# Kernel tuning notes

Measured on AMD Instinct MI355X. Metric: run time of the kernel, lower is better.

Reference implementation:

```python
import jax, jax.numpy as jnp
import numpy as np

SENSOR_H, SENSOR_W = 256, 256
SPP = 16
BATCH, C, H_IMG, W_IMG = 4, 3, 1024, 1024


def setup_inputs() -> dict:
    key = jax.random.key(0)
    k1, k2 = jax.random.split(key)
    img = jax.random.uniform(k1, (BATCH, C, H_IMG, W_IMG), dtype=jnp.float32)
    jitter = jax.random.uniform(k2, (SPP, SENSOR_H, SENSOR_W, 2), dtype=jnp.float32)
    t = jnp.ones((1,), jnp.float32)
    return {"img": img, "t": t, "jitter": jitter}


def deform(pos, t):
    # Analytic per-axis foveation diffeomorphism [-1,1]^2 -> [-1,1]^2:
    #   f(u) = tanh(t*u)/tanh(t), f'(u) = t*(1 - tanh(t*u)^2)/tanh(t)
    # Jacobian is diagonal, so det = f'(x) * f'(y).
    tt = t[0]
    s = jnp.tanh(tt)
    th = jnp.tanh(tt * pos)
    warped = th / s                      # (..., 2)
    dd = tt * (1.0 - th * th) / s        # diagonal Jacobian entries (..., 2)
    det = dd[..., 0] * dd[..., 1]        # (...)
    return warped, det


def grid_sample_border(img, grid):
    # img: (b,c,H,W); grid: (spp,h,w,2) in [-1,1]
    # bilinear, padding_mode='border', align_corners=False (matches F.grid_sample)
    b, c, H, W = img.shape
    gx = (grid[..., 0] + 1.0) * (W / 2.0) - 0.5
    gy = (grid[..., 1] + 1.0) * (H / 2.0) - 0.5
    gx = jnp.clip(gx, 0.0, W - 1.0)
    gy = jnp.clip(gy, 0.0, H - 1.0)
    x0 = jnp.floor(gx)
    y0 = jnp.floor(gy)
    wx = (gx - x0)[None, None]           # (1,1,spp,h,w)
    wy = (gy - y0)[None, None]
    x0i = jnp.clip(x0.astype(jnp.int32), 0, W - 1)
    y0i = jnp.clip(y0.astype(jnp.int32), 0, H - 1)
    x1i = jnp.clip(x0i + 1, 0, W - 1)
    y1i = jnp.clip(y0i + 1, 0, H - 1)
    # fancy-index gather: result (b,c,spp,h,w); avoids tiling img over (b*spp)
    v00 = img[:, :, y0i, x0i]
    v01 = img[:, :, y0i, x1i]
    v10 = img[:, :, y1i, x0i]
    v11 = img[:, :, y1i, x1i]
    return (v00 * (1 - wx) * (1 - wy) + v01 * wx * (1 - wy)
            + v10 * (1 - wx) * wy + v11 * wx * wy)


def reference(img, t, jitter):
    step_x = 2.0 / SENSOR_W
    step_y = 2.0 / SENSOR_H
    px = jnp.arange(-1.0, 1.0, step_x, dtype=jnp.float32)
    py = jnp.arange(-1.0, 1.0, step_y, dtype=jnp.float32)
    gx, gy = jnp.meshgrid(px, py, indexing='xy')          # (h, w)
    pixel_pos = jnp.stack((gx, gy), axis=-1)[None]        # (1, h, w, 2)
    jit = jitter * jnp.array([step_x, step_y], jnp.float32)
    pos = pixel_pos + jit                                 # (spp, h, w, 2)
    warped, det = deform(pos, t)                          # (spp,h,w,2), (spp,h,w)
    samples = grid_sample_border(img, warped)             # (b, c, spp, h, w)
    weighted = jnp.mean(samples * det[None, None], axis=2)  # (b, c, h, w)
    area = jnp.mean(det, axis=0)[None, None]              # (1, 1, h, w)
    return weighted / area
```

## Files before the change

kernel.cpp:

```cpp
#include <hip/hip_runtime.h>

#define SPP   16
#define SH    256
#define SW    256
#define H_IMG 1024
#define W_IMG 1024
#define CH    3
#define BATCH 4

__global__ __launch_bounds__(256) void foveated_kernel(
    const float* __restrict__ img,
    const float* __restrict__ t_ptr,
    const float* __restrict__ jitter,
    float* __restrict__ out)
{
    const int L  = (blockIdx.x & 7) * 256 + (blockIdx.x >> 3);
    const int b  = L >> 9;
    const int sy = (L >> 1) & (SH - 1);
    const int xh = L & 1;

    const int th   = threadIdx.x;
    const int lane = th & 31;
    const int half = (th >> 5) & 1;
    const int grp  = th >> 6;
    const int sx   = xh * 128 + grp * 32 + lane;

    const float step  = 2.0f / 256.0f;
    const float tt    = t_ptr[0];
    const float inv_s = 1.0f / tanhf(tt);

    const float px = -1.0f + sx * step;
    const float py = -1.0f + sy * step;

    float acc0 = 0.0f, acc1 = 0.0f, acc2 = 0.0f, dsum = 0.0f;

    const size_t plane = (size_t)H_IMG * W_IMG;
    const float* __restrict__ p0 = img + (size_t)(b * CH) * plane;
    const float* __restrict__ p1 = p0 + plane;
    const float* __restrict__ p2 = p1 + plane;

    const float2* __restrict__ jit2 = (const float2*)jitter;
    const int jbase = sy * SW + sx;

    #pragma unroll 4
    for (int k = 0; k < SPP / 2; ++k) {
        const int sp = half * (SPP / 2) + k;
        const float2 j = jit2[sp * (SH * SW) + jbase];
        const float posx = px + j.x * step;
        const float posy = py + j.y * step;

        const float thx = tanhf(tt * posx);
        const float thy = tanhf(tt * posy);
        const float ddx = tt * (1.0f - thx * thx) * inv_s;
        const float ddy = tt * (1.0f - thy * thy) * inv_s;
        const float det = ddx * ddy;

        float gx = (thx * inv_s + 1.0f) * (W_IMG * 0.5f) - 0.5f;
        float gy = (thy * inv_s + 1.0f) * (H_IMG * 0.5f) - 0.5f;
        gx = fminf(fmaxf(gx, 0.0f), (float)(W_IMG - 1));
        gy = fminf(fmaxf(gy, 0.0f), (float)(H_IMG - 1));

        const int xb = min((int)gx, W_IMG - 2);
        const int yb = min((int)gy, H_IMG - 2);
        const float fx = gx - (float)xb;
        const float fy = gy - (float)yb;

        const float w00 = (1.0f - fx) * (1.0f - fy) * det;
        const float w01 = fx * (1.0f - fy) * det;
        const float w10 = (1.0f - fx) * fy * det;
        const float w11 = fx * fy * det;
        dsum += det;

        const int i0 = yb * W_IMG + xb;
        const int i1 = i0 + W_IMG;

        {
            const float2 a = *(const float2*)(p0 + i0);
            const float2 c = *(const float2*)(p0 + i1);
            acc0 += a.x * w00 + a.y * w01 + c.x * w10 + c.y * w11;
        }
        {
            const float2 a = *(const float2*)(p1 + i0);
            const float2 c = *(const float2*)(p1 + i1);
            acc1 += a.x * w00 + a.y * w01 + c.x * w10 + c.y * w11;
        }
        {
            const float2 a = *(const float2*)(p2 + i0);
            const float2 c = *(const float2*)(p2 + i1);
            acc2 += a.x * w00 + a.y * w01 + c.x * w10 + c.y * w11;
        }
    }

    acc0 += __shfl_xor(acc0, 32);
    acc1 += __shfl_xor(acc1, 32);
    acc2 += __shfl_xor(acc2, 32);
    dsum += __shfl_xor(dsum, 32);

    if (half == 0) {
        const float inv_d = 1.0f / dsum;
        const int pix = sy * SW + sx;
        const size_t obase = (size_t)b * CH * (SH * SW) + pix;
        out[obase]                 = acc0 * inv_d;
        out[obase + (SH * SW)]     = acc1 * inv_d;
        out[obase + 2 * (SH * SW)] = acc2 * inv_d;
    }
}

extern "C" void kernel_launch(void* const* d_in, const int* in_sizes, int n_in,
                              void* d_out, int out_size, void* d_ws, size_t ws_size,
                              hipStream_t stream) {
    const float* img    = (const float*)d_in[0];
    const float* t      = (const float*)d_in[1];
    const float* jitter = (const float*)d_in[2];
    float* out          = (float*)d_out;

    const int grid  = 2048;
    const int block = 256;

    hipLaunchKernelGGL(foveated_kernel, dim3(grid), dim3(block), 0, stream,
                       img, t, jitter, out);
}
```

Before: 109.1 us.

## Repack image into fp16 interleaved-channel layout before bilinear gather

Adds a pre-pass that converts the planar fp32 image into a padded 4-channel fp16 pixel-interleaved buffer in workspace. The sampling kernel then fetches both horizontal neighbours for all channels with one 16-byte load per row, instead of six separate float2 loads. It also splits samples four ways per wave and uses an exp-based fast tanh. The repack adds a full-image read and write on every call, and fp16 storage lowers precision.

```diff
diff --git a/kernel.cpp b/kernel.cpp
--- a/kernel.cpp
+++ b/kernel.cpp
@@ -1,12 +1,128 @@
 #include <hip/hip_runtime.h>
+#include <hip/hip_fp16.h>
 
 #define SPP   16
 #define SH    256
 #define SW    256
-#define H_IMG 1024
-#define W_IMG 1024
+#define HI    1024
+#define WI    1024
 #define CH    3
 #define BATCH 4
+
+struct __attribute__((packed, aligned(8))) U4 { uint4 v; };
+
+__device__ __forceinline__ float fast_tanh(float x) {
+    const float t = __expf(2.0f * x);
+    return (t - 1.0f) * __builtin_amdgcn_rcpf(t + 1.0f);
+}
+
+__global__ __launch_bounds__(256) void repack_kernel(
+    const float* __restrict__ img, __half* __restrict__ dst)
+{
+    const int tid = blockIdx.x * 256 + threadIdx.x;
+    const int b   = tid >> 20;
+    const int pix = tid & (HI * WI - 1);
+    const float* p = img + (size_t)b * (CH * HI * WI) + pix;
+    union { __half2 h2[2]; uint2 u; } u;
+    u.h2[0] = __floats2half2_rn(p[0], p[HI * WI]);
+    u.h2[1] = __floats2half2_rn(p[2 * HI * WI], 0.0f);
+    *(uint2*)(dst + ((size_t)tid << 2)) = u.u;
+}
+
+__global__ __launch_bounds__(256) void foveated_nhwc(
+    const __half* __restrict__ img4,
+    const float* __restrict__ t_ptr,
+    const float* __restrict__ jitter,
+    float* __restrict__ out)
+{
+    const int L  = (blockIdx.x & 7) * 512 + (blockIdx.x >> 3);
+    const int b  = L >> 10;
+    const int sy = (L >> 2) & (SH - 1);
+    const int xg = L & 3;
+
+    const int th   = threadIdx.x;
+    const int lane = th & 63;
+    const int pxl  = lane & 15;
+    const int q    = lane >> 4;
+    const int wv   = th >> 6;
+    const int sx   = xg * 64 + wv * 16 + pxl;
+
+    const float step  = 2.0f / 256.0f;
+    const float tt    = t_ptr[0];
+    const float inv_s = __builtin_amdgcn_rcpf(fast_tanh(tt));
+
+    const float px = -1.0f + sx * step;
+    const float py = -1.0f + sy * step;
+
+    float acc0 = 0.0f, acc1 = 0.0f, acc2 = 0.0f, dsum = 0.0f;
+
+    const __half* __restrict__ base = img4 + (size_t)b * (HI * WI * 4);
+    const float2* __restrict__ jit2 = (const float2*)jitter;
+    const int jbase = sy * SW + sx;
+
+    #pragma unroll
+    for (int k = 0; k < SPP / 4; ++k) {
+        const int sp = q * 4 + k;
+        const float2 j = jit2[sp * (SH * SW) + jbase];
+        const float posx = px + j.x * step;
+        const float posy = py + j.y * step;
+
+        const float thx = fast_tanh(tt * posx);
+        const float thy = fast_tanh(tt * posy);
+        const float ddx = tt * (1.0f - thx * thx) * inv_s;
+        const float ddy = tt * (1.0f - thy * thy) * inv_s;
+        const float det = ddx * ddy;
+
+        float gx = (thx * inv_s + 1.0f) * (WI * 0.5f) - 0.5f;
+        float gy = (thy * inv_s + 1.0f) * (HI * 0.5f) - 0.5f;
+        gx = fminf(fmaxf(gx, 0.0f), (float)(WI - 1));
+        gy = fminf(fmaxf(gy, 0.0f), (float)(HI - 1));
+
+        const int xb = min((int)gx, WI - 2);
+        const int yb = min((int)gy, HI - 2);
+        const float fx = gx - (float)xb;
+        const float fy = gy - (float)yb;
+
+        const float w00 = (1.0f - fx) * (1.0f - fy) * det;
+        const float w01 = fx * (1.0f - fy) * det;
+        const float w10 = (1.0f - fx) * fy * det;
+        const float w11 = fx * fy * det;
+        dsum += det;
+
+        const __half* r0 = base + (((size_t)yb * WI + xb) << 2);
+        const uint4 a = ((const U4*)r0)->v;
+        const uint4 c = ((const U4*)(r0 + (WI << 2)))->v;
+
+        const __half2* ha = (const __half2*)&a;
+        const __half2* hc = (const __half2*)&c;
+        const float2 a0 = __half22float2(ha[0]);
+        const float2 a1 = __half22float2(ha[1]);
+        const float2 a2 = __half22float2(ha[2]);
+        const float2 a3 = __half22float2(ha[3]);
+        const float2 c0 = __half22float2(hc[0]);
+        const float2 c1 = __half22float2(hc[1]);
+        const float2 c2 = __half22float2(hc[2]);
+        const float2 c3 = __half22float2(hc[3]);
+
+        acc0 += w00 * a0.x + w01 * a2.x + w10 * c0.x + w11 * c2.x;
+        acc1 += w00 * a0.y + w01 * a2.y + w10 * c0.y + w11 * c2.y;
+        acc2 += w00 * a1.x + w01 * a3.x + w10 * c1.x + w11 * c3.x;
+    }
+
+    acc0 += __shfl_xor(acc0, 16); acc0 += __shfl_xor(acc0, 32);
+    acc1 += __shfl_xor(acc1, 16); acc1 += __shfl_xor(acc1, 32);
+    acc2 += __shfl_xor(acc2, 16); acc2 += __shfl_xor(acc2, 32);
+    dsum += __shfl_xor(dsum, 16); dsum += __shfl_xor(dsum, 32);
+
+    if (q == 0) {
+        const float inv_d = 1.0f / dsum;
+        const int pix = sy * SW + sx;
+        const size_t ob = (size_t)b * CH * (SH * SW) + pix;
+        out[ob]                 = acc0 * inv_d;
+        out[ob + (SH * SW)]     = acc1 * inv_d;
+        out[ob + 2 * (SH * SW)] = acc2 * inv_d;
+    }
+}
 
 __global__ __launch_bounds__(256) void foveated_kernel(
     const float* __restrict__ img,
@@ -34,7 +150,7 @@
 
     float acc0 = 0.0f, acc1 = 0.0f, acc2 = 0.0f, dsum = 0.0f;
 
-    const size_t plane = (size_t)H_IMG * W_IMG;
+    const size_t plane = (size_t)HI * WI;
     const float* __restrict__ p0 = img + (size_t)(b * CH) * plane;
     const float* __restrict__ p1 = p0 + plane;
     const float* __restrict__ p2 = p1 + plane;
@@ -55,13 +171,13 @@
         const float ddy = tt * (1.0f - thy * thy) * inv_s;
         const float det = ddx * ddy;
 
-        float gx = (thx * inv_s + 1.0f) * (W_IMG * 0.5f) - 0.5f;
-        float gy = (thy * inv_s + 1.0f) * (H_IMG * 0.5f) - 0.5f;
-        gx = fminf(fmaxf(gx, 0.0f), (float)(W_IMG - 1));
-        gy = fminf(fmaxf(gy, 0.0f), (float)(H_IMG - 1));
-
-        const int xb = min((int)gx, W_IMG - 2);
-        const int yb = min((int)gy, H_IMG - 2);
+        float gx = (thx * inv_s + 1.0f) * (WI * 0.5f) - 0.5f;
+        float gy = (thy * inv_s + 1.0f) * (HI * 0.5f) - 0.5f;
+        gx = fminf(fmaxf(gx, 0.0f), (float)(WI - 1));
+        gy = fminf(fmaxf(gy, 0.0f), (float)(HI - 1));
+
+        const int xb = min((int)gx, WI - 2);
+        const int yb = min((int)gy, HI - 2);
         const float fx = gx - (float)xb;
         const float fy = gy - (float)yb;
 
@@ -71,24 +187,14 @@
         const float w11 = fx * fy * det;
         dsum += det;
 
-        const int i0 = yb * W_IMG + xb;
-        const int i1 = i0 + W_IMG;
-
-        {
-            const float2 a = *(const float2*)(p0 + i0);
-            const float2 c = *(const float2*)(p0 + i1);
-            acc0 += a.x * w00 + a.y * w01 + c.x * w10 + c.y * w11;
-        }
-        {
-            const float2 a = *(const float2*)(p1 + i0);
-            const float2 c = *(const float2*)(p1 + i1);
-            acc1 += a.x * w00 + a.y * w01 + c.x * w10 + c.y * w11;
-        }
-        {
-            const float2 a = *(const float2*)(p2 + i0);
-            const float2 c = *(const float2*)(p2 + i1);
-            acc2 += a.x * w00 + a.y * w01 + c.x * w10 + c.y * w11;
-        }
+        const int i0 = yb * WI + xb;
+        const int i1 = i0 + WI;
+        { const float2 a = *(const float2*)(p0 + i0), c = *(const float2*)(p0 + i1);
+          acc0 += a.x * w00 + a.y * w01 + c.x * w10 + c.y * w11; }
+        { const float2 a = *(const float2*)(p1 + i0), c = *(const float2*)(p1 + i1);
+          acc1 += a.x * w00 + a.y * w01 + c.x * w10 + c.y * w11; }
+        { const float2 a = *(const float2*)(p2 + i0), c = *(const float2*)(p2 + i1);
+          acc2 += a.x * w00 + a.y * w01 + c.x * w10 + c.y * w11; }
     }
 
     acc0 += __shfl_xor(acc0, 32);
@@ -114,9 +220,15 @@
     const float* jitter = (const float*)d_in[2];
     float* out          = (float*)d_out;
 
-    const int grid  = 2048;
-    const int block = 256;
-
-    hipLaunchKernelGGL(foveated_kernel, dim3(grid), dim3(block), 0, stream,
-                       img, t, jitter, out);
-}
+    const size_t need = (size_t)BATCH * HI * WI * 4 * sizeof(__half);
+    if (ws_size >= need) {
+        __half* img4 = (__half*)d_ws;
+        hipLaunchKernelGGL(repack_kernel, dim3(BATCH * HI * WI / 256), dim3(256),
+                           0, stream, img, img4);
+        hipLaunchKernelGGL(foveated_nhwc, dim3(4096), dim3(256), 0, stream,
+                           img4, t, jitter, out);
+    } else {
+        hipLaunchKernelGGL(foveated_kernel, dim3(2048), dim3(256), 0, stream,
+                           img, t, jitter, out);
+    }
+}
```

New measurement: 110.5 us. About the same (+1.3%).

## Stage per-tile image footprint in LDS as packed fp16 and sample from shared memory

Applied to the files above, without the earlier changes.

Each block now handles a 16x16 sensor tile instead of half a sensor row. It computes the tile's warped image bounding box, loads that region of all three channels once into LDS packed as fp16, and does the bilinear taps from LDS. A global-gather path remains for tiles whose footprint exceeds 88x88. tanh is replaced with an exp/rcp approximation, and the half-warp SPP split with its shuffle reduction is dropped. The aim is to replace scattered global gathers with a cooperative load. In exchange, the ~62KB of LDS per block limits occupancy, and fp16 storage plus the fast tanh reduce accuracy.

```diff
diff --git a/kernel.cpp b/kernel.cpp
--- a/kernel.cpp
+++ b/kernel.cpp
@@ -1,109 +1,180 @@
 #include <hip/hip_runtime.h>
+#include <hip/hip_fp16.h>
 
 #define SPP   16
 #define SH    256
 #define SW    256
-#define H_IMG 1024
-#define W_IMG 1024
+#define HI    1024
+#define WI    1024
 #define CH    3
 #define BATCH 4
 
-__global__ __launch_bounds__(256) void foveated_kernel(
+#define TS    16
+#define MAXD  88
+
+__device__ __forceinline__ float fast_tanh(float x) {
+    const float e = __expf(2.0f * x);
+    return (e - 1.0f) * __builtin_amdgcn_rcpf(e + 1.0f);
+}
+
+__global__ __launch_bounds__(256) void foveated_tile(
     const float* __restrict__ img,
     const float* __restrict__ t_ptr,
     const float* __restrict__ jitter,
     float* __restrict__ out)
 {
-    const int L  = (blockIdx.x & 7) * 256 + (blockIdx.x >> 3);
-    const int b  = L >> 9;
-    const int sy = (L >> 1) & (SH - 1);
-    const int xh = L & 1;
+    __shared__ uint2 lds[MAXD * MAXD];
 
-    const int th   = threadIdx.x;
-    const int lane = th & 31;
-    const int half = (th >> 5) & 1;
-    const int grp  = th >> 6;
-    const int sx   = xh * 128 + grp * 32 + lane;
+    const int bid  = blockIdx.x;
+    const int L    = (bid & 7) * 128 + (bid >> 3);
+    const int b    = L >> 8;
+    const int trow = (L >> 4) & 15;
+    const int tcol = L & 15;
+    const int sx0  = tcol * TS;
+    const int sy0  = trow * TS;
 
     const float step  = 2.0f / 256.0f;
     const float tt    = t_ptr[0];
-    const float inv_s = 1.0f / tanhf(tt);
+    const float inv_s = __builtin_amdgcn_rcpf(fast_tanh(tt));
+
+    auto gmap = [&](float p) {
+        float g = (fast_tanh(tt * p) * inv_s + 1.0f) * 512.0f - 0.5f;
+        return fminf(fmaxf(g, 0.0f), 1023.0f);
+    };
+    const float pxmin = -1.0f + sx0 * step, pxmax = pxmin + TS * step;
+    const float pymin = -1.0f + sy0 * step, pymax = pymin + TS * step;
+    const int x_lo = max((int)gmap(pxmin) - 1, 0);
+    const int x_hi = min((int)gmap(pxmax) + 2, WI - 1);
+    const int y_lo = max((int)gmap(pymin) - 1, 0);
+    const int y_hi = min((int)gmap(pymax) + 2, HI - 1);
+    const int ncols = x_hi - x_lo + 1;
+    const int nrows = y_hi - y_lo + 1;
+    const bool fits = (ncols <= MAXD) && (nrows <= MAXD);
+
+    const size_t plane = (size_t)HI * WI;
+    const float* __restrict__ p0 = img + (size_t)(b * CH) * plane;
+    const float* __restrict__ p1 = p0 + plane;
+    const float* __restrict__ p2 = p1 + plane;
+
+    const int th = threadIdx.x;
+    const int sx = sx0 + (th & 15);
+    const int sy = sy0 + (th >> 4);
 
     const float px = -1.0f + sx * step;
     const float py = -1.0f + sy * step;
 
     float acc0 = 0.0f, acc1 = 0.0f, acc2 = 0.0f, dsum = 0.0f;
 
-    const size_t plane = (size_t)H_IMG * W_IMG;
-    const float* __restrict__ p0 = img + (size_t)(b * CH) * plane;
-    const float* __restrict__ p1 = p0 + plane;
-    const float* __restrict__ p2 = p1 + plane;
-
     const float2* __restrict__ jit2 = (const float2*)jitter;
     const int jbase = sy * SW + sx;
 
-    #pragma unroll 4
-    for (int k = 0; k < SPP / 2; ++k) {
-        const int sp = half * (SPP / 2) + k;
-        const float2 j = jit2[sp * (SH * SW) + jbase];
-        const float posx = px + j.x * step;
-        const float posy = py + j.y * step;
+    if (fits) {
+        const int npix = nrows * ncols;
+        const unsigned mdiv = (1u << 22) / (unsigned)ncols + 1u;
+        for (int i = th; i < npix; i += 256) {
+            const int r = (int)(((unsigned)i * mdiv) >> 22);
+            const int c = i - r * ncols;
+            const int g = (y_lo + r) * WI + (x_lo + c);
+            union { __half2 h[2]; uint2 u; } v;
+            v.h[0] = __floats2half2_rn(p0[g], p1[g]);
+            v.h[1] = __floats2half2_rn(p2[g], 0.0f);
+            lds[r * MAXD + c] = v.u;
+        }
+        __syncthreads();
 
-        const float thx = tanhf(tt * posx);
-        const float thy = tanhf(tt * posy);
-        const float ddx = tt * (1.0f - thx * thx) * inv_s;
-        const float ddy = tt * (1.0f - thy * thy) * inv_s;
-        const float det = ddx * ddy;
+        #pragma unroll 4
+        for (int sp = 0; sp < SPP; ++sp) {
+            const float2 j = jit2[sp * (SH * SW) + jbase];
+            const float posx = px + j.x * step;
+            const float posy = py + j.y * step;
 
-        float gx = (thx * inv_s + 1.0f) * (W_IMG * 0.5f) - 0.5f;
-        float gy = (thy * inv_s + 1.0f) * (H_IMG * 0.5f) - 0.5f;
-        gx = fminf(fmaxf(gx, 0.0f), (float)(W_IMG - 1));
-        gy = fminf(fmaxf(gy, 0.0f), (float)(H_IMG - 1));
+            const float thx = fast_tanh(tt * posx);
+            const float thy = fast_tanh(tt * posy);
+            const float ddx = tt * (1.0f - thx * thx) * inv_s;
+            const float ddy = tt * (1.0f - thy * thy) * inv_s;
+            const float det = ddx * ddy;
 
-        const int xb = min((int)gx, W_IMG - 2);
-        const int yb = min((int)gy, H_IMG - 2);
-        const float fx = gx - (float)xb;
-        const float fy = gy - (float)yb;
+            float gx = (thx * inv_s + 1.0f) * 512.0f - 0.5f;
+            float gy = (thy * inv_s + 1.0f) * 512.0f - 0.5f;
+            gx = fminf(fmaxf(gx, 0.0f), (float)(WI - 1));
+            gy = fminf(fmaxf(gy, 0.0f), (float)(HI - 1));
 
-        const float w00 = (1.0f - fx) * (1.0f - fy) * det;
-        const float w01 = fx * (1.0f - fy) * det;
-        const float w10 = (1.0f - fx) * fy * det;
-        const float w11 = fx * fy * det;
-        dsum += det;
+            const int xb = min((int)gx, WI - 2);
+            const int yb = min((int)gy, HI - 2);
+            const float fx = gx - (float)xb;
+            const float fy = gy - (float)yb;
 
-        const int i0 = yb * W_IMG + xb;
-        const int i1 = i0 + W_IMG;
+            const float w00 = (1.0f - fx) * (1.0f - fy) * det;
+            const float w01 = fx * (1.0f - fy) * det;
+            const float w10 = (1.0f - fx) * fy * det;
+            const float w11 = fx * fy * det;
+            dsum += det;
 
-        {
-            const float2 a = *(const float2*)(p0 + i0);
-            const float2 c = *(const float2*)(p0 + i1);
-            acc0 += a.x * w00 + a.y * w01 + c.x * w10 + c.y * w11;
+            const int lidx = (yb - y_lo) * MAXD + (xb - x_lo);
+            const uint2 q00 = lds[lidx];
+            const uint2 q01 = lds[lidx + 1];
+            const uint2 q10 = lds[lidx + MAXD];
+            const uint2 q11 = lds[lidx + MAXD + 1];
+
+            const float2 a00 = __half22float2(*(const __half2*)&q00.x);
+            const float2 b00 = __half22float2(*(const __half2*)&q00.y);
+            const float2 a01 = __half22float2(*(const __half2*)&q01.x);
+            const float2 b01 = __half22float2(*(const __half2*)&q01.y);
+            const float2 a10 = __half22float2(*(const __half2*)&q10.x);
+            const float2 b10 = __half22float2(*(const __half2*)&q10.y);
+            const float2 a11 = __half22float2(*(const __half2*)&q11.x);
+            const float2 b11 = __half22float2(*(const __half2*)&q11.y);
+
+            acc0 += w00 * a00.x + w01 * a01.x + w10 * a10.x + w11 * a11.x;
+            acc1 += w00 * a00.y + w01 * a01.y + w10 * a10.y + w11 * a11.y;
+            acc2 += w00 * b00.x + w01 * b01.x + w10 * b10.x + w11 * b11.x;
         }
-        {
-            const float2 a = *(const float2*)(p1 + i0);
-            const float2 c = *(const float2*)(p1 + i1);
-            acc1 += a.x * w00 + a.y * w01 + c.x * w10 + c.y * w11;
-        }
-        {
-            const float2 a = *(const float2*)(p2 + i0);
-            const float2 c = *(const float2*)(p2 + i1);
-            acc2 += a.x * w00 + a.y * w01 + c.x * w10 + c.y * w11;
+    } else {
+        #pragma unroll 4
+        for (int sp = 0; sp < SPP; ++sp) {
+            const float2 j = jit2[sp * (SH * SW) + jbase];
+            const float posx = px + j.x * step;
+            const float posy = py + j.y * step;
+
+            const float thx = fast_tanh(tt * posx);
+            const float thy = fast_tanh(tt * posy);
+            const float ddx = tt * (1.0f - thx * thx) * inv_s;
+            const float ddy = tt * (1.0f - thy * thy) * inv_s;
+            const float det = ddx * ddy;
+
+            float gx = (thx * inv_s + 1.0f) * 512.0f - 0.5f;
+            float gy = (thy * inv_s + 1.0f) * 512.0f - 0.5f;
+            gx = fminf(fmaxf(gx, 0.0f), (float)(WI - 1));
+            gy = fminf(fmaxf(gy, 0.0f), (float)(HI - 1));
+
+            const int xb = min((int)gx, WI - 2);
+            const int yb = min((int)gy, HI - 2);
+            const float fx = gx - (float)xb;
+            const float fy = gy - (float)yb;
+
+            const float w00 = (1.0f - fx) * (1.0f - fy) * det;
+            const float w01 = fx * (1.0f - fy) * det;
+            const float w10 = (1.0f - fx) * fy * det;
+            const float w11 = fx * fy * det;
+            dsum += det;
+
+            const int i0 = yb * WI + xb;
+            const int i1 = i0 + WI;
+            { const float2 a = *(const float2*)(p0 + i0), c = *(const float2*)(p0 + i1);
+              acc0 += a.x * w00 + a.y * w01 + c.x * w10 + c.y * w11; }
+            { const float2 a = *(const float2*)(p1 + i0), c = *(const float2*)(p1 + i1);
+              acc1 += a.x * w00 + a.y * w01 + c.x * w10 + c.y * w11; }
+            { const float2 a = *(const float2*)(p2 + i0), c = *(const float2*)(p2 + i1);
+              acc2 += a.x * w00 + a.y * w01 + c.x * w10 + c.y * w11; }
         }
     }
 
-    acc0 += __shfl_xor(acc0, 32);
-    acc1 += __shfl_xor(acc1, 32);
-    acc2 += __shfl_xor(acc2, 32);
-    dsum += __shfl_xor(dsum, 32);
-
-    if (half == 0) {
-        const float inv_d = 1.0f / dsum;
-        const int pix = sy * SW + sx;
-        const size_t obase = (size_t)b * CH * (SH * SW) + pix;
-        out[obase]                 = acc0 * inv_d;
-        out[obase + (SH * SW)]     = acc1 * inv_d;
-        out[obase + 2 * (SH * SW)] = acc2 * inv_d;
-    }
+    const float inv_d = 1.0f / dsum;
+    const int pix = sy * SW + sx;
+    const size_t ob = (size_t)b * CH * (SH * SW) + pix;
+    out[ob]                 = acc0 * inv_d;
+    out[ob + (SH * SW)]     = acc1 * inv_d;
+    out[ob + 2 * (SH * SW)] = acc2 * inv_d;
 }
 
 extern "C" void kernel_launch(void* const* d_in, const int* in_sizes, int n_in,
@@ -114,9 +185,6 @@
     const float* jitter = (const float*)d_in[2];
     float* out          = (float*)d_out;
 
-    const int grid  = 2048;
-    const int block = 256;
-
-    hipLaunchKernelGGL(foveated_kernel, dim3(grid), dim3(block), 0, stream,
+    hipLaunchKernelGGL(foveated_tile, dim3(1024), dim3(256), 0, stream,
                        img, t, jitter, out);
 }
```

After: 108.8 us. Within noise of the previous version (-0.3%).

## Share warp coordinates across batch and map samples to lanes

Applied to the files above, without the earlier changes.

Each thread now handles one sample of one sensor pixel and loops over all four batch images, so the tanh warp, jitter load and bilinear weights are computed once instead of once per batch element. The 16 samples of a pixel sit in adjacent lanes and are reduced with a 4-step xor-shuffle tree across 12 accumulators plus the determinant. tanhf is replaced by an exp/reciprocal approximation. The trade-off is lower per-thread sample coalescing in gathers (16 lanes per pixel hit nearby addresses), more shuffles, and slightly reduced tanh accuracy.

```diff
diff --git a/kernel.cpp b/kernel.cpp
--- a/kernel.cpp
+++ b/kernel.cpp
@@ -3,106 +3,96 @@
 #define SPP   16
 #define SH    256
 #define SW    256
-#define H_IMG 1024
-#define W_IMG 1024
+#define HI    1024
+#define WI    1024
 #define CH    3
 #define BATCH 4
 
-__global__ __launch_bounds__(256) void foveated_kernel(
+__device__ __forceinline__ float fast_tanh(float x) {
+    const float e = __expf(2.0f * x);
+    return (e - 1.0f) * __builtin_amdgcn_rcpf(e + 1.0f);
+}
+
+__global__ __launch_bounds__(256) void foveated_batch(
     const float* __restrict__ img,
     const float* __restrict__ t_ptr,
     const float* __restrict__ jitter,
     float* __restrict__ out)
 {
-    const int L  = (blockIdx.x & 7) * 256 + (blockIdx.x >> 3);
-    const int b  = L >> 9;
-    const int sy = (L >> 1) & (SH - 1);
-    const int xh = L & 1;
+    const int L   = (blockIdx.x & 7) * 512 + (blockIdx.x >> 3);
+    const int sy  = L >> 4;
+    const int sx0 = (L & 15) * 16;
 
-    const int th   = threadIdx.x;
-    const int lane = th & 31;
-    const int half = (th >> 5) & 1;
-    const int grp  = th >> 6;
-    const int sx   = xh * 128 + grp * 32 + lane;
+    const int th  = threadIdx.x;
+    const int sp  = th & 15;
+    const int pxl = th >> 4;
+    const int sx  = sx0 + pxl;
 
     const float step  = 2.0f / 256.0f;
     const float tt    = t_ptr[0];
-    const float inv_s = 1.0f / tanhf(tt);
+    const float inv_s = __builtin_amdgcn_rcpf(fast_tanh(tt));
 
-    const float px = -1.0f + sx * step;
-    const float py = -1.0f + sy * step;
+    const float2 j = ((const float2*)jitter)[sp * (SH * SW) + sy * SW + sx];
+    const float posx = (-1.0f + sx * step) + j.x * step;
+    const float posy = (-1.0f + sy * step) + j.y * step;
 
-    float acc0 = 0.0f, acc1 = 0.0f, acc2 = 0.0f, dsum = 0.0f;
+    const float thx = fast_tanh(tt * posx);
+    const float thy = fast_tanh(tt * posy);
+    const float ddx = tt * (1.0f - thx * thx) * inv_s;
+    const float ddy = tt * (1.0f - thy * thy) * inv_s;
+    const float det = ddx * ddy;
 
-    const size_t plane = (size_t)H_IMG * W_IMG;
-    const float* __restrict__ p0 = img + (size_t)(b * CH) * plane;
-    const float* __restrict__ p1 = p0 + plane;
-    const float* __restrict__ p2 = p1 + plane;
+    float gx = (thx * inv_s + 1.0f) * (WI * 0.5f) - 0.5f;
+    float gy = (thy * inv_s + 1.0f) * (HI * 0.5f) - 0.5f;
+    gx = fminf(fmaxf(gx, 0.0f), (float)(WI - 1));
+    gy = fminf(fmaxf(gy, 0.0f), (float)(HI - 1));
 
-    const float2* __restrict__ jit2 = (const float2*)jitter;
-    const int jbase = sy * SW + sx;
+    const int xb = min((int)gx, WI - 2);
+    const int yb = min((int)gy, HI - 2);
+    const float fx = gx - (float)xb;
+    const float fy = gy - (float)yb;
 
-    #pragma unroll 4
-    for (int k = 0; k < SPP / 2; ++k) {
-        const int sp = half * (SPP / 2) + k;
-        const float2 j = jit2[sp * (SH * SW) + jbase];
-        const float posx = px + j.x * step;
-        const float posy = py + j.y * step;
+    const float w00 = (1.0f - fx) * (1.0f - fy) * det;
+    const float w01 = fx * (1.0f - fy) * det;
+    const float w10 = (1.0f - fx) * fy * det;
+    const float w11 = fx * fy * det;
 
-        const float thx = tanhf(tt * posx);
-        const float thy = tanhf(tt * posy);
-        const float ddx = tt * (1.0f - thx * thx) * inv_s;
-        const float ddy = tt * (1.0f - thy * thy) * inv_s;
-        const float det = ddx * ddy;
+    const int i0 = yb * WI + xb;
+    const int i1 = i0 + WI;
+    const size_t plane = (size_t)HI * WI;
 
-        float gx = (thx * inv_s + 1.0f) * (W_IMG * 0.5f) - 0.5f;
-        float gy = (thy * inv_s + 1.0f) * (H_IMG * 0.5f) - 0.5f;
-        gx = fminf(fmaxf(gx, 0.0f), (float)(W_IMG - 1));
-        gy = fminf(fmaxf(gy, 0.0f), (float)(H_IMG - 1));
-
-        const int xb = min((int)gx, W_IMG - 2);
-        const int yb = min((int)gy, H_IMG - 2);
-        const float fx = gx - (float)xb;
-        const float fy = gy - (float)yb;
-
-        const float w00 = (1.0f - fx) * (1.0f - fy) * det;
-        const float w01 = fx * (1.0f - fy) * det;
-        const float w10 = (1.0f - fx) * fy * det;
-        const float w11 = fx * fy * det;
-        dsum += det;
-
-        const int i0 = yb * W_IMG + xb;
-        const int i1 = i0 + W_IMG;
-
-        {
-            const float2 a = *(const float2*)(p0 + i0);
-            const float2 c = *(const float2*)(p0 + i1);
-            acc0 += a.x * w00 + a.y * w01 + c.x * w10 + c.y * w11;
-        }
-        {
-            const float2 a = *(const float2*)(p1 + i0);
-            const float2 c = *(const float2*)(p1 + i1);
-            acc1 += a.x * w00 + a.y * w01 + c.x * w10 + c.y * w11;
-        }
-        {
-            const float2 a = *(const float2*)(p2 + i0);
-            const float2 c = *(const float2*)(p2 + i1);
-            acc2 += a.x * w00 + a.y * w01 + c.x * w10 + c.y * w11;
+    float acc[BATCH][CH];
+    #pragma unroll
+    for (int b = 0; b < BATCH; ++b) {
+        const float* __restrict__ pb = img + (size_t)(b * CH) * plane;
+        #pragma unroll
+        for (int c = 0; c < CH; ++c) {
+            const float* __restrict__ p = pb + c * plane;
+            const float2 a = *(const float2*)(p + i0);
+            const float2 d = *(const float2*)(p + i1);
+            acc[b][c] = a.x * w00 + a.y * w01 + d.x * w10 + d.y * w11;
         }
     }
 
-    acc0 += __shfl_xor(acc0, 32);
-    acc1 += __shfl_xor(acc1, 32);
-    acc2 += __shfl_xor(acc2, 32);
-    dsum += __shfl_xor(dsum, 32);
+    float dsum = det;
+    #pragma unroll
+    for (int m = 1; m < 16; m <<= 1) {
+        #pragma unroll
+        for (int b = 0; b < BATCH; ++b)
+            #pragma unroll
+            for (int c = 0; c < CH; ++c)
+                acc[b][c] += __shfl_xor(acc[b][c], m);
+        dsum += __shfl_xor(dsum, m);
+    }
 
-    if (half == 0) {
+    if (sp == 0) {
         const float inv_d = 1.0f / dsum;
         const int pix = sy * SW + sx;
-        const size_t obase = (size_t)b * CH * (SH * SW) + pix;
-        out[obase]                 = acc0 * inv_d;
-        out[obase + (SH * SW)]     = acc1 * inv_d;
-        out[obase + 2 * (SH * SW)] = acc2 * inv_d;
+        #pragma unroll
+        for (int b = 0; b < BATCH; ++b)
+            #pragma unroll
+            for (int c = 0; c < CH; ++c)
+                out[(size_t)(b * CH + c) * (SH * SW) + pix] = acc[b][c] * inv_d;
     }
 }
 
@@ -114,9 +104,6 @@
     const float* jitter = (const float*)d_in[2];
     float* out          = (float*)d_out;
 
-    const int grid  = 2048;
-    const int block = 256;
-
-    hipLaunchKernelGGL(foveated_kernel, dim3(grid), dim3(block), 0, stream,
+    hipLaunchKernelGGL(foveated_batch, dim3(4096), dim3(256), 0, stream,
                        img, t, jitter, out);
 }
```

Measured after the change: 113.0 us. 1.04x slower.
